# Optimization experiments

Measured on AMD Instinct MI355X. Metric: run time of the kernel, lower is better.

## Reference

```python
import jax, jax.numpy as jnp
import numpy as np

NBINS = 30
LO, HI = -6.0, 6.0
BINWIDTH = (HI - LO) / (NBINS - 2)  # interior bin width, matches abs((hi-lo)/(nbins-2))


def setup_inputs() -> dict:
    key = jax.random.key(0)
    x = jax.random.normal(key, (4096, 16384), dtype=jnp.float32)
    return {"x": x}


def reference(x):
    # Single-pass digitize + scatter-add, mathematically identical to the
    # original per-bin threshold-compare loop:
    #   bin 0 (orig BinPop[1]):      x <  LO
    #   bin i (orig BinPop[i+1]):    LO+(i-1)*w <= x < LO+i*w, i=1..nbins-2
    #   bin nbins-1 (BinPop[nbins]): x >= HI   (HI == LO + (nbins-2)*w)
    b, n = x.shape
    k = jnp.clip(jnp.floor((x - LO) / BINWIDTH), -1.0, NBINS - 2).astype(jnp.int32) + 1
    rows = jnp.arange(b, dtype=jnp.int32)[:, None]  # [b,1] broadcast against [b,n]
    hist_nat = jnp.zeros((b, NBINS), dtype=x.dtype).at[rows, k].add(1.0)
    # The original concatenates dict values in insertion order:
    # [bin1, bin_nbins, bin2, ..., bin_{nbins-1}]
    order = np.concatenate([[0], [NBINS - 1], np.arange(1, NBINS - 1)])
    return hist_nat[:, order]
```

## Files before the change

kernel.cpp:

```cpp
#include <hip/hip_runtime.h>


#define NBINS   30
#define THREADS 256
#define ROWLEN  16384
#define VPG     4
#define GROUPS  (ROWLEN / 4 / THREADS / VPG)

typedef float f4 __attribute__((ext_vector_type(4)));

__global__ __launch_bounds__(THREADS) void hist_kernel(
    const float* __restrict__ x, float* __restrict__ out)
{
    __shared__ unsigned int h[NBINS * THREADS];
    __shared__ unsigned int partial[8 * NBINS];

    const int t   = threadIdx.x;
    const int row = blockIdx.x;

#pragma unroll
    for (int b = 0; b < NBINS; ++b) h[b * THREADS + t] = 0u;
    __syncthreads();

    const float invW = 28.0f / 12.0f;
    const float c15  = 15.0f;

    const f4* xr = (const f4*)(x + (size_t)row * ROWLEN);

    f4 cur[VPG], nxt[VPG];
#pragma unroll
    for (int j = 0; j < VPG; ++j)
        cur[j] = __builtin_nontemporal_load(&xr[t + j * THREADS]);

#pragma unroll 1
    for (int g = 0; g < GROUPS; ++g) {
        if (g + 1 < GROUPS) {
#pragma unroll
            for (int j = 0; j < VPG; ++j)
                nxt[j] = __builtin_nontemporal_load(
                    &xr[t + ((g + 1) * VPG + j) * THREADS]);
        }
#pragma unroll
        for (int j = 0; j < VPG; ++j) {
            f4 v = cur[j];
#pragma unroll
            for (int c = 0; c < 4; ++c) {
                float f = fmaf(v[c], invW, c15);
                f = fminf(fmaxf(f, 0.0f), 29.0f);
                int bin = __float2int_rd(f);
                atomicAdd(&h[bin * THREADS + t], 1u);
            }
        }
#pragma unroll
        for (int j = 0; j < VPG; ++j) cur[j] = nxt[j];
    }
    __syncthreads();

    if (t < 240) {
        const int b = t % NBINS;
        const int g = t / NBINS;
        unsigned int s = 0;
#pragma unroll
        for (int i = 0; i < 32; ++i)
            s += h[b * THREADS + g * 32 + ((i + b) & 31)];
        partial[g * NBINS + b] = s;
    }
    __syncthreads();

    if (t < NBINS) {
        unsigned int s = 0;
#pragma unroll
        for (int g = 0; g < 8; ++g) s += partial[g * NBINS + t];
        const int dst = (t == 0) ? 0 : (t == NBINS - 1) ? 1 : (t + 1);
        out[(size_t)row * NBINS + dst] = (float)s;
    }
}

extern "C" void kernel_launch(void* const* d_in, const int* in_sizes, int n_in,
                              void* d_out, int out_size, void* d_ws, size_t ws_size,
                              hipStream_t stream)
{
    const float* x  = (const float*)d_in[0];
    float* out      = (float*)d_out;
    const int rows  = in_sizes[0] / ROWLEN;
    hist_kernel<<<rows, THREADS, 0, stream>>>(x, out);
}
```

Before: 330.0 us.

## Replace LDS atomic histogram with wave-ballot cumulative threshold counts

Drops the per-thread shared-memory histogram and its LDS atomics. Each value is instead compared against all 29 bin thresholds, and a wave ballot plus popcount accumulates a wave-uniform cumulative count for each threshold. Bin counts are then recovered as differences of adjacent cumulative counts after a small cross-wave reduction. This removes LDS contention and the shared-memory zeroing, at the cost of 29 compares and ballots per element.

```diff
diff --git a/kernel.cpp b/kernel.cpp
--- a/kernel.cpp
+++ b/kernel.cpp
@@ -2,6 +2,7 @@
 
 
 #define NBINS   30
+#define NCDF    29
 #define THREADS 256
 #define ROWLEN  16384
 #define VPG     4
@@ -12,20 +13,19 @@
 __global__ __launch_bounds__(THREADS) void hist_kernel(
     const float* __restrict__ x, float* __restrict__ out)
 {
-    __shared__ unsigned int h[NBINS * THREADS];
-    __shared__ unsigned int partial[8 * NBINS];
+    __shared__ unsigned int wc[4][NCDF];
 
     const int t   = threadIdx.x;
     const int row = blockIdx.x;
-
-#pragma unroll
-    for (int b = 0; b < NBINS; ++b) h[b * THREADS + t] = 0u;
-    __syncthreads();
 
     const float invW = 28.0f / 12.0f;
     const float c15  = 15.0f;
 
     const f4* xr = (const f4*)(x + (size_t)row * ROWLEN);
+
+    unsigned int cnt[NCDF];
+#pragma unroll
+    for (int i = 0; i < NCDF; ++i) cnt[i] = 0u;
 
     f4 cur[VPG], nxt[VPG];
 #pragma unroll
@@ -46,33 +46,32 @@
 #pragma unroll
             for (int c = 0; c < 4; ++c) {
                 float f = fmaf(v[c], invW, c15);
-                f = fminf(fmaxf(f, 0.0f), 29.0f);
-                int bin = __float2int_rd(f);
-                atomicAdd(&h[bin * THREADS + t], 1u);
+#pragma unroll
+                for (int i = 0; i < NCDF; ++i)
+                    cnt[i] += (unsigned int)__popcll(
+                        __ballot(f < (float)(i + 1)));
             }
         }
 #pragma unroll
         for (int j = 0; j < VPG; ++j) cur[j] = nxt[j];
     }
-    __syncthreads();
 
-    if (t < 240) {
-        const int b = t % NBINS;
-        const int g = t / NBINS;
-        unsigned int s = 0;
+    if ((t & 63) == 0) {
+        const int w = t >> 6;
 #pragma unroll
-        for (int i = 0; i < 32; ++i)
-            s += h[b * THREADS + g * 32 + ((i + b) & 31)];
-        partial[g * NBINS + b] = s;
+        for (int i = 0; i < NCDF; ++i) wc[w][i] = cnt[i];
     }
     __syncthreads();
 
     if (t < NBINS) {
-        unsigned int s = 0;
-#pragma unroll
-        for (int g = 0; g < 8; ++g) s += partial[g * NBINS + t];
+        unsigned int hi = (t < NCDF)
+            ? (wc[0][t] + wc[1][t] + wc[2][t] + wc[3][t])
+            : (unsigned int)ROWLEN;
+        unsigned int lo = (t == 0)
+            ? 0u
+            : (wc[0][t - 1] + wc[1][t - 1] + wc[2][t - 1] + wc[3][t - 1]);
         const int dst = (t == 0) ? 0 : (t == NBINS - 1) ? 1 : (t + 1);
-        out[(size_t)row * NBINS + dst] = (float)s;
+        out[(size_t)row * NBINS + dst] = (float)(hi - lo);
     }
 }
 
```

New measurement: 422.8 us. +28.1%, slower.
